# Performance work log

Hardware: AMD Instinct MI355X
Metric: run time of the kernel (lower is better)

## Reference

```python
import jax, jax.numpy as jnp
import numpy as np

DELTA_V = 0.5
DELTA_D = 3.0
ALPHA = 1.0
BETA = 1.0
GAMMA = 0.001
K = 5  # max instance label (labels 1..K; 0 = background)


def setup_inputs() -> dict:
    key = jax.random.key(0)
    k1, k2 = jax.random.split(key)
    B, D, H, W = 8, 8, 512, 1024
    embedding = jax.random.normal(k1, (B, D, H, W), dtype=jnp.float32)
    instance_mask = jax.random.randint(k2, (B, H, W), 0, K + 1, dtype=jnp.int32)
    return {"embedding": embedding, "instance_mask": instance_mask}


def _disc_loss(embedding, instance_mask):
    B, D, H, W = embedding.shape
    P = H * W
    emb = embedding.transpose(0, 2, 3, 1).reshape(B, P, D)      # [B,P,D]
    labels = instance_mask.reshape(B, P)                         # [B,P]

    # one-hot over instance labels 1..K (background excluded)
    onehot = (labels[..., None] == jnp.arange(1, K + 1, dtype=labels.dtype)).astype(emb.dtype)  # [B,P,K]
    counts = onehot.sum(axis=1)                                  # [B,K]
    present = counts > 0                                         # [B,K]
    presentf = present.astype(emb.dtype)
    N = presentf.sum(axis=-1)                                    # [B] num instances

    # per-instance centers via segment mean
    sums = jnp.einsum('bpd,bpk->bkd', emb, onehot)               # [B,K,D]
    centers = sums / jnp.maximum(counts, 1.0)[..., None]         # [B,K,D]

    # ---- variance loss: per-pixel distance to own center ----
    idx = jnp.clip(labels - 1, 0, K - 1)                         # [B,P]
    c_pix = jnp.take_along_axis(centers, idx[..., None], axis=1) # [B,P,D]
    d = jnp.sqrt(jnp.sum((emb - c_pix) ** 2, axis=-1))           # [B,P]
    val = jnp.maximum(d - DELTA_V, 0.0) ** 2                     # [B,P]
    inst_sum = jnp.einsum('bp,bpk->bk', val, onehot)             # [B,K]
    inst_mean = inst_sum / jnp.maximum(counts, 1.0)
    loss_var_b = (inst_mean * presentf).sum(-1) / jnp.maximum(N, 1.0)  # [B]

    # ---- distance loss: pairwise center hinge ----
    diff = centers[:, :, None, :] - centers[:, None, :, :]       # [B,K,K,D]
    dist_sq = jnp.sum(diff ** 2, axis=-1)                        # [B,K,K]
    iu = jnp.triu(jnp.ones((K, K), dtype=bool), k=1)             # i<j
    pair_mask = present[:, :, None] & present[:, None, :] & iu   # [B,K,K]
    safe_dist = jnp.sqrt(jnp.where(pair_mask, dist_sq, 1.0))
    term = jnp.maximum(2.0 * DELTA_D - safe_dist, 0.0) ** 2 * pair_mask.astype(emb.dtype)
    n_pairs = N * (N - 1.0) / 2.0
    loss_dist_b = term.sum((-1, -2)) / jnp.where(N > 1, n_pairs, 1.0)  # [B]

    # ---- regularization: mean norm of present centers ----
    c_norm = jnp.sqrt(jnp.where(present, jnp.sum(centers ** 2, axis=-1), 1.0))
    loss_reg_b = (c_norm * presentf).sum(-1) / jnp.maximum(N, 1.0)     # [B]

    # ---- batch mean over images that have at least one instance ----
    has = (N > 0).astype(emb.dtype)                              # [B]
    denom = jnp.maximum(has.sum(), 1.0)
    loss_var = (loss_var_b * has).sum() / denom
    loss_dist = (loss_dist_b * has).sum() / denom
    loss_reg = (loss_reg_b * has).sum() / denom
    total = ALPHA * loss_var + BETA * loss_dist + GAMMA * loss_reg
    return (total, loss_var, loss_dist, loss_reg)


def reference(embedding, instance_mask):
    return _disc_loss(embedding, instance_mask)
```

## Files before the change

kernel.cpp:

```cpp
#include <hip/hip_runtime.h>
#include <math.h>

constexpr int NB   = 8;
constexpr int ND   = 8;
constexpr int NH   = 512;
constexpr int NW   = 1024;
constexpr int NP   = NH * NW;
constexpr int NG   = NP / 4;
constexpr int NK   = 5;
constexpr int BPB  = 128;
constexpr int GPB  = NG / BPB;
constexpr int NVAL = NK * ND + NK;

constexpr float DELTA_V = 0.5f;
constexpr float TWO_DELTA_D = 6.0f;
constexpr float GAMMA = 0.001f;

__device__ __forceinline__ float wave_sum(float v) {
#pragma unroll
    for (int off = 32; off > 0; off >>= 1) v += __shfl_down(v, off, 64);
    return v;
}

__global__ __launch_bounds__(256) void pass1_kernel(const float* __restrict__ emb,
                                                    const int* __restrict__ mask,
                                                    float* __restrict__ sums,
                                                    float* __restrict__ cnts) {
    const int b   = blockIdx.x / BPB;
    const int blk = blockIdx.x % BPB;
    const long base = (long)blk * GPB;

    const float4* emb4 = (const float4*)emb;
    const int4*   m4p  = (const int4*)mask + (long)b * NG;

    float acc[NK][ND];
    float cnt[NK];
#pragma unroll
    for (int k = 0; k < NK; ++k) {
        cnt[k] = 0.f;
#pragma unroll
        for (int d = 0; d < ND; ++d) acc[k][d] = 0.f;
    }

    for (int it = threadIdx.x; it < GPB; it += blockDim.x) {
        const long g = base + it;
        const int4 m = m4p[g];
        float4 e[ND];
#pragma unroll
        for (int d = 0; d < ND; ++d)
            e[d] = emb4[((long)(b * ND + d)) * NG + g];
        const int labs[4] = {m.x, m.y, m.z, m.w};
#pragma unroll
        for (int j = 0; j < 4; ++j) {
            const int lab = labs[j];
#pragma unroll
            for (int k = 0; k < NK; ++k) {
                const float is = (lab == k + 1) ? 1.f : 0.f;
                cnt[k] += is;
#pragma unroll
                for (int d = 0; d < ND; ++d)
                    acc[k][d] = fmaf(is, ((const float*)&e[d])[j], acc[k][d]);
            }
        }
    }

    __shared__ float part[4][NVAL];
    const int lane = threadIdx.x & 63;
    const int wave = threadIdx.x >> 6;
#pragma unroll
    for (int k = 0; k < NK; ++k) {
#pragma unroll
        for (int d = 0; d < ND; ++d) {
            const float r = wave_sum(acc[k][d]);
            if (lane == 0) part[wave][k * ND + d] = r;
        }
        const float rc = wave_sum(cnt[k]);
        if (lane == 0) part[wave][NK * ND + k] = rc;
    }
    __syncthreads();
    if (threadIdx.x < NVAL) {
        const float s = part[0][threadIdx.x] + part[1][threadIdx.x] +
                        part[2][threadIdx.x] + part[3][threadIdx.x];
        if (threadIdx.x < NK * ND)
            atomicAdd(&sums[b * NK * ND + threadIdx.x], s);
        else
            atomicAdd(&cnts[b * NK + (threadIdx.x - NK * ND)], s);
    }
}

__global__ __launch_bounds__(256) void pass2_kernel(const float* __restrict__ emb,
                                                    const int* __restrict__ mask,
                                                    const float* __restrict__ sums,
                                                    const float* __restrict__ cnts,
                                                    float* __restrict__ vsums) {
    const int b   = blockIdx.x / BPB;
    const int blk = blockIdx.x % BPB;
    const long base = (long)blk * GPB;

    float c[NK][ND];
#pragma unroll
    for (int k = 0; k < NK; ++k) {
        const float inv = 1.f / fmaxf(cnts[b * NK + k], 1.f);
#pragma unroll
        for (int d = 0; d < ND; ++d)
            c[k][d] = sums[b * NK * ND + k * ND + d] * inv;
    }

    const float4* emb4 = (const float4*)emb;
    const int4*   m4p  = (const int4*)mask + (long)b * NG;

    float vacc[NK] = {0.f, 0.f, 0.f, 0.f, 0.f};

    for (int it = threadIdx.x; it < GPB; it += blockDim.x) {
        const long g = base + it;
        const int4 m = m4p[g];
        float4 e[ND];
#pragma unroll
        for (int d = 0; d < ND; ++d)
            e[d] = emb4[((long)(b * ND + d)) * NG + g];
        const int labs[4] = {m.x, m.y, m.z, m.w};
#pragma unroll
        for (int j = 0; j < 4; ++j) {
            const int lab = labs[j];
            float dsq = 0.f;
#pragma unroll
            for (int d = 0; d < ND; ++d) {
                float cd = c[0][d];
                cd = (lab == 2) ? c[1][d] : cd;
                cd = (lab == 3) ? c[2][d] : cd;
                cd = (lab == 4) ? c[3][d] : cd;
                cd = (lab == 5) ? c[4][d] : cd;
                const float diff = ((const float*)&e[d])[j] - cd;
                dsq = fmaf(diff, diff, dsq);
            }
            const float dist = sqrtf(dsq);
            float hv = fmaxf(dist - DELTA_V, 0.f);
            const float val = hv * hv;
#pragma unroll
            for (int k = 0; k < NK; ++k)
                vacc[k] += (lab == k + 1) ? val : 0.f;
        }
    }

    __shared__ float part[4][NK];
    const int lane = threadIdx.x & 63;
    const int wave = threadIdx.x >> 6;
#pragma unroll
    for (int k = 0; k < NK; ++k) {
        const float r = wave_sum(vacc[k]);
        if (lane == 0) part[wave][k] = r;
    }
    __syncthreads();
    if (threadIdx.x < NK) {
        const float s = part[0][threadIdx.x] + part[1][threadIdx.x] +
                        part[2][threadIdx.x] + part[3][threadIdx.x];
        atomicAdd(&vsums[b * NK + threadIdx.x], s);
    }
}

__global__ void final_kernel(const float* __restrict__ sums,
                             const float* __restrict__ cnts,
                             const float* __restrict__ vsums,
                             float* __restrict__ out) {
    if (threadIdx.x != 0 || blockIdx.x != 0) return;
    float tv = 0.f, td = 0.f, tr = 0.f, hs = 0.f;
    for (int b = 0; b < NB; ++b) {
        float cnt[NK];
        bool  pres[NK];
        float c[NK][ND];
        float N = 0.f;
        for (int k = 0; k < NK; ++k) {
            cnt[k]  = cnts[b * NK + k];
            pres[k] = cnt[k] > 0.f;
            if (pres[k]) N += 1.f;
            const float inv = 1.f / fmaxf(cnt[k], 1.f);
            for (int d = 0; d < ND; ++d)
                c[k][d] = sums[b * NK * ND + k * ND + d] * inv;
        }
        float lv = 0.f;
        for (int k = 0; k < NK; ++k)
            if (pres[k]) lv += vsums[b * NK + k] / fmaxf(cnt[k], 1.f);
        lv /= fmaxf(N, 1.f);
        float ld = 0.f;
        for (int i = 0; i < NK; ++i)
            for (int j = i + 1; j < NK; ++j)
                if (pres[i] && pres[j]) {
                    float dsq = 0.f;
                    for (int d = 0; d < ND; ++d) {
                        const float df = c[i][d] - c[j][d];
                        dsq = fmaf(df, df, dsq);
                    }
                    const float t = fmaxf(TWO_DELTA_D - sqrtf(dsq), 0.f);
                    ld += t * t;
                }
        const float npairs = N * (N - 1.f) * 0.5f;
        ld /= (N > 1.f) ? npairs : 1.f;
        float lr = 0.f;
        for (int k = 0; k < NK; ++k)
            if (pres[k]) {
                float sq = 0.f;
                for (int d = 0; d < ND; ++d) sq = fmaf(c[k][d], c[k][d], sq);
                lr += sqrtf(sq);
            }
        lr /= fmaxf(N, 1.f);

        if (N > 0.f) { tv += lv; td += ld; tr += lr; hs += 1.f; }
    }
    const float denom = fmaxf(hs, 1.f);
    tv /= denom; td /= denom; tr /= denom;
    out[0] = tv + td + GAMMA * tr;
    out[1] = tv;
    out[2] = td;
    out[3] = tr;
}

extern "C" void kernel_launch(void* const* d_in, const int* in_sizes, int n_in,
                              void* d_out, int out_size, void* d_ws, size_t ws_size,
                              hipStream_t stream) {
    const float* emb  = (const float*)d_in[0];
    const int*   mask = (const int*)d_in[1];
    float* out = (float*)d_out;

    float* sums  = (float*)d_ws;
    float* cnts  = sums + NB * NK * ND;
    float* vsums = cnts + NB * NK;

    hipMemsetAsync(d_ws, 0, (size_t)(NB * NK * ND + 2 * NB * NK) * sizeof(float), stream);

    dim3 grid(NB * BPB), block(256);
    pass1_kernel<<<grid, block, 0, stream>>>(emb, mask, sums, cnts);
    pass2_kernel<<<grid, block, 0, stream>>>(emb, mask, sums, cnts, vsums);
    final_kernel<<<1, 64, 0, stream>>>(sums, cnts, vsums, out);
}
```

Baseline: 284.2 us.

## Fuse both passes and finalization into one persistent kernel with grid barriers

Replaces the memset plus three kernel launches with a single 512-block kernel. Block 0 zeroes the workspace in-kernel, and the other blocks wait on a ready flag. Software grid barriers separate the center-accumulation pass, the variance pass and the final scalar reduction, and the pixel loops are fully unrolled with a fixed trip count. The aim is to remove launch and memset overhead and to let the second read of the embedding hit the on-chip caches. In exchange it relies on all blocks being co-resident. The ready flag persists across calls, so a later call could race with the workspace reset.

```diff
diff --git a/kernel.cpp b/kernel.cpp
--- a/kernel.cpp
+++ b/kernel.cpp
@@ -1,20 +1,24 @@
 #include <hip/hip_runtime.h>
 #include <math.h>
 
-constexpr int NB   = 8;
-constexpr int ND   = 8;
-constexpr int NH   = 512;
-constexpr int NW   = 1024;
-constexpr int NP   = NH * NW;
-constexpr int NG   = NP / 4;
-constexpr int NK   = 5;
-constexpr int BPB  = 128;
+constexpr int NB = 8, ND = 8, NH = 512, NW = 1024;
+constexpr int NP = NH * NW;
+constexpr int NG = NP / 4;
+constexpr int NK = 5;
+constexpr int NBLK = 512;
+constexpr int BPB  = NBLK / NB;
 constexpr int GPB  = NG / BPB;
+constexpr int ITER = GPB / 256;
 constexpr int NVAL = NK * ND + NK;
 
 constexpr float DELTA_V = 0.5f;
 constexpr float TWO_DELTA_D = 6.0f;
 constexpr float GAMMA = 0.001f;
+constexpr int READY_MAGIC = 0x13572468;
+
+#define SCOPE __HIP_MEMORY_SCOPE_AGENT
+
+constexpr int WS_INTS = 416;
 
 __device__ __forceinline__ float wave_sum(float v) {
 #pragma unroll
@@ -22,19 +26,48 @@
     return v;
 }
 
-__global__ __launch_bounds__(256) void pass1_kernel(const float* __restrict__ emb,
-                                                    const int* __restrict__ mask,
-                                                    float* __restrict__ sums,
-                                                    float* __restrict__ cnts) {
+__device__ __forceinline__ void grid_barrier(int* cnt, int* gen) {
+    __syncthreads();
+    if (threadIdx.x == 0) {
+        const int g = __hip_atomic_load(gen, __ATOMIC_ACQUIRE, SCOPE);
+        const int t = __hip_atomic_fetch_add(cnt, 1, __ATOMIC_ACQ_REL, SCOPE);
+        if (t == NBLK - 1) {
+            __hip_atomic_store(cnt, 0, __ATOMIC_RELAXED, SCOPE);
+            __hip_atomic_fetch_add(gen, 1, __ATOMIC_ACQ_REL, SCOPE);
+        } else {
+            while (__hip_atomic_load(gen, __ATOMIC_ACQUIRE, SCOPE) == g)
+                __builtin_amdgcn_s_sleep(2);
+        }
+    }
+    __syncthreads();
+}
+
+__global__ __launch_bounds__(256, 2) void disc_fused(
+    const float* __restrict__ emb, const int* __restrict__ mask,
+    int* __restrict__ wsi, float* __restrict__ out)
+{
+    float* const sums    = (float*)(wsi + 16);
+    float* const cnts    = sums + NB * NK * ND;
+    float* const vsums   = cnts + NB * NK;
+    int* const   bar_cnt = wsi + 0;
+    int* const   bar_gen = wsi + 1;
+    int* const   ready   = wsi + 2;
+
     const int b   = blockIdx.x / BPB;
     const int blk = blockIdx.x % BPB;
     const long base = (long)blk * GPB;
-
-    const float4* emb4 = (const float4*)emb;
+    const float4* emb4 = (const float4*)emb + (long)b * ND * NG;
     const int4*   m4p  = (const int4*)mask + (long)b * NG;
 
-    float acc[NK][ND];
-    float cnt[NK];
+    if (blockIdx.x == 0) {
+        for (int i = threadIdx.x; i < WS_INTS; i += 256)
+            __hip_atomic_store(wsi + i, 0, __ATOMIC_RELAXED, SCOPE);
+        __syncthreads();
+        if (threadIdx.x == 0)
+            __hip_atomic_store(ready, READY_MAGIC, __ATOMIC_RELEASE, SCOPE);
+    }
+
+    float acc[NK][ND], cnt[NK];
 #pragma unroll
     for (int k = 0; k < NK; ++k) {
         cnt[k] = 0.f;
@@ -42,24 +75,24 @@
         for (int d = 0; d < ND; ++d) acc[k][d] = 0.f;
     }
 
-    for (int it = threadIdx.x; it < GPB; it += blockDim.x) {
-        const long g = base + it;
+#pragma unroll
+    for (int i = 0; i < ITER; ++i) {
+        const long g = base + threadIdx.x + i * 256;
         const int4 m = m4p[g];
         float4 e[ND];
 #pragma unroll
-        for (int d = 0; d < ND; ++d)
-            e[d] = emb4[((long)(b * ND + d)) * NG + g];
+        for (int d = 0; d < ND; ++d) e[d] = emb4[(long)d * NG + g];
         const int labs[4] = {m.x, m.y, m.z, m.w};
 #pragma unroll
         for (int j = 0; j < 4; ++j) {
             const int lab = labs[j];
 #pragma unroll
             for (int k = 0; k < NK; ++k) {
-                const float is = (lab == k + 1) ? 1.f : 0.f;
-                cnt[k] += is;
+                const bool sel = (lab == k + 1);
+                cnt[k] += sel ? 1.f : 0.f;
 #pragma unroll
                 for (int d = 0; d < ND; ++d)
-                    acc[k][d] = fmaf(is, ((const float*)&e[d])[j], acc[k][d]);
+                    acc[k][d] += sel ? ((const float*)&e[d])[j] : 0.f;
             }
         }
     }
@@ -77,47 +110,45 @@
         const float rc = wave_sum(cnt[k]);
         if (lane == 0) part[wave][NK * ND + k] = rc;
     }
+    if (threadIdx.x == 0 && blockIdx.x != 0) {
+        while (__hip_atomic_load(ready, __ATOMIC_ACQUIRE, SCOPE) != READY_MAGIC)
+            __builtin_amdgcn_s_sleep(2);
+    }
     __syncthreads();
     if (threadIdx.x < NVAL) {
         const float s = part[0][threadIdx.x] + part[1][threadIdx.x] +
                         part[2][threadIdx.x] + part[3][threadIdx.x];
-        if (threadIdx.x < NK * ND)
-            atomicAdd(&sums[b * NK * ND + threadIdx.x], s);
-        else
-            atomicAdd(&cnts[b * NK + (threadIdx.x - NK * ND)], s);
-    }
-}
-
-__global__ __launch_bounds__(256) void pass2_kernel(const float* __restrict__ emb,
-                                                    const int* __restrict__ mask,
-                                                    const float* __restrict__ sums,
-                                                    const float* __restrict__ cnts,
-                                                    float* __restrict__ vsums) {
-    const int b   = blockIdx.x / BPB;
-    const int blk = blockIdx.x % BPB;
-    const long base = (long)blk * GPB;
-
+        float* dst = (threadIdx.x < NK * ND)
+                         ? &sums[b * NK * ND + threadIdx.x]
+                         : &cnts[b * NK + (threadIdx.x - NK * ND)];
+        atomicAdd(dst, s);
+    }
+    grid_barrier(bar_cnt, bar_gen);
+
+    __shared__ float csh[NVAL];
+    if (threadIdx.x < NVAL) {
+        const float* src = (threadIdx.x < NK * ND)
+                               ? &sums[b * NK * ND + threadIdx.x]
+                               : &cnts[b * NK + (threadIdx.x - NK * ND)];
+        csh[threadIdx.x] = __hip_atomic_load(src, __ATOMIC_RELAXED, SCOPE);
+    }
+    __syncthreads();
     float c[NK][ND];
 #pragma unroll
     for (int k = 0; k < NK; ++k) {
-        const float inv = 1.f / fmaxf(cnts[b * NK + k], 1.f);
-#pragma unroll
-        for (int d = 0; d < ND; ++d)
-            c[k][d] = sums[b * NK * ND + k * ND + d] * inv;
-    }
-
-    const float4* emb4 = (const float4*)emb;
-    const int4*   m4p  = (const int4*)mask + (long)b * NG;
+        const float inv = 1.f / fmaxf(csh[NK * ND + k], 1.f);
+#pragma unroll
+        for (int d = 0; d < ND; ++d) c[k][d] = csh[k * ND + d] * inv;
+    }
 
     float vacc[NK] = {0.f, 0.f, 0.f, 0.f, 0.f};
-
-    for (int it = threadIdx.x; it < GPB; it += blockDim.x) {
-        const long g = base + it;
+#pragma unroll
+    for (int i = 0; i < ITER; ++i) {
+        const long g = base + threadIdx.x + i * 256;
         const int4 m = m4p[g];
         float4 e[ND];
 #pragma unroll
-        for (int d = 0; d < ND; ++d)
-            e[d] = emb4[((long)(b * ND + d)) * NG + g];
+        for (int d = 0; d < ND; ++d) e[d] = emb4[(long)d * NG + g];
         const int labs[4] = {m.x, m.y, m.z, m.w};
 #pragma unroll
         for (int j = 0; j < 4; ++j) {
@@ -134,17 +165,13 @@
                 dsq = fmaf(diff, diff, dsq);
             }
             const float dist = sqrtf(dsq);
-            float hv = fmaxf(dist - DELTA_V, 0.f);
+            const float hv = fmaxf(dist - DELTA_V, 0.f);
             const float val = hv * hv;
 #pragma unroll
             for (int k = 0; k < NK; ++k)
                 vacc[k] += (lab == k + 1) ? val : 0.f;
         }
     }
-
-    __shared__ float part[4][NK];
-    const int lane = threadIdx.x & 63;
-    const int wave = threadIdx.x >> 6;
 #pragma unroll
     for (int k = 0; k < NK; ++k) {
         const float r = wave_sum(vacc[k]);
@@ -156,62 +183,63 @@
                         part[2][threadIdx.x] + part[3][threadIdx.x];
         atomicAdd(&vsums[b * NK + threadIdx.x], s);
     }
-}
-
-__global__ void final_kernel(const float* __restrict__ sums,
-                             const float* __restrict__ cnts,
-                             const float* __restrict__ vsums,
-                             float* __restrict__ out) {
-    if (threadIdx.x != 0 || blockIdx.x != 0) return;
-    float tv = 0.f, td = 0.f, tr = 0.f, hs = 0.f;
-    for (int b = 0; b < NB; ++b) {
-        float cnt[NK];
-        bool  pres[NK];
-        float c[NK][ND];
-        float N = 0.f;
-        for (int k = 0; k < NK; ++k) {
-            cnt[k]  = cnts[b * NK + k];
-            pres[k] = cnt[k] > 0.f;
-            if (pres[k]) N += 1.f;
-            const float inv = 1.f / fmaxf(cnt[k], 1.f);
-            for (int d = 0; d < ND; ++d)
-                c[k][d] = sums[b * NK * ND + k * ND + d] * inv;
-        }
-        float lv = 0.f;
-        for (int k = 0; k < NK; ++k)
-            if (pres[k]) lv += vsums[b * NK + k] / fmaxf(cnt[k], 1.f);
-        lv /= fmaxf(N, 1.f);
-        float ld = 0.f;
-        for (int i = 0; i < NK; ++i)
-            for (int j = i + 1; j < NK; ++j)
-                if (pres[i] && pres[j]) {
-                    float dsq = 0.f;
-                    for (int d = 0; d < ND; ++d) {
-                        const float df = c[i][d] - c[j][d];
-                        dsq = fmaf(df, df, dsq);
+    grid_barrier(bar_cnt, bar_gen);
+
+    if (blockIdx.x == 0 && threadIdx.x == 0) {
+        float tv = 0.f, td = 0.f, tr = 0.f, hs = 0.f;
+        for (int bb = 0; bb < NB; ++bb) {
+            float cc[NK], CC[NK][ND];
+            bool pres[NK];
+            float N = 0.f;
+            for (int k = 0; k < NK; ++k) {
+                cc[k] = __hip_atomic_load(&cnts[bb * NK + k], __ATOMIC_RELAXED, SCOPE);
+                pres[k] = cc[k] > 0.f;
+                if (pres[k]) N += 1.f;
+                const float inv = 1.f / fmaxf(cc[k], 1.f);
+                for (int d = 0; d < ND; ++d)
+                    CC[k][d] = __hip_atomic_load(&sums[bb * NK * ND + k * ND + d],
+                                                 __ATOMIC_RELAXED, SCOPE) * inv;
+            }
+            float lv = 0.f;
+            for (int k = 0; k < NK; ++k)
+                if (pres[k])
+                    lv += __hip_atomic_load(&vsums[bb * NK + k], __ATOMIC_RELAXED, SCOPE)
+                          / fmaxf(cc[k], 1.f);
+            lv /= fmaxf(N, 1.f);
+
+            float ld = 0.f;
+            for (int i2 = 0; i2 < NK; ++i2)
+                for (int j2 = i2 + 1; j2 < NK; ++j2)
+                    if (pres[i2] && pres[j2]) {
+                        float dsq = 0.f;
+                        for (int d = 0; d < ND; ++d) {
+                            const float df = CC[i2][d] - CC[j2][d];
+                            dsq = fmaf(df, df, dsq);
+                        }
+                        const float t = fmaxf(TWO_DELTA_D - sqrtf(dsq), 0.f);
+                        ld += t * t;
                     }
-                    const float t = fmaxf(TWO_DELTA_D - sqrtf(dsq), 0.f);
-                    ld += t * t;
+            const float npairs = N * (N - 1.f) * 0.5f;
+            ld /= (N > 1.f) ? npairs : 1.f;
+
+            float lr = 0.f;
+            for (int k = 0; k < NK; ++k)
+                if (pres[k]) {
+                    float sq = 0.f;
+                    for (int d = 0; d < ND; ++d) sq = fmaf(CC[k][d], CC[k][d], sq);
+                    lr += sqrtf(sq);
                 }
-        const float npairs = N * (N - 1.f) * 0.5f;
-        ld /= (N > 1.f) ? npairs : 1.f;
-        float lr = 0.f;
-        for (int k = 0; k < NK; ++k)
-            if (pres[k]) {
-                float sq = 0.f;
-                for (int d = 0; d < ND; ++d) sq = fmaf(c[k][d], c[k][d], sq);
-                lr += sqrtf(sq);
-            }
-        lr /= fmaxf(N, 1.f);
-
-        if (N > 0.f) { tv += lv; td += ld; tr += lr; hs += 1.f; }
-    }
-    const float denom = fmaxf(hs, 1.f);
-    tv /= denom; td /= denom; tr /= denom;
-    out[0] = tv + td + GAMMA * tr;
-    out[1] = tv;
-    out[2] = td;
-    out[3] = tr;
+            lr /= fmaxf(N, 1.f);
+
+            if (N > 0.f) { tv += lv; td += ld; tr += lr; hs += 1.f; }
+        }
+        const float den = fmaxf(hs, 1.f);
+        tv /= den; td /= den; tr /= den;
+        out[0] = tv + td + GAMMA * tr;
+        out[1] = tv;
+        out[2] = td;
+        out[3] = tr;
+    }
 }
 
 extern "C" void kernel_launch(void* const* d_in, const int* in_sizes, int n_in,
@@ -219,16 +247,5 @@
                               hipStream_t stream) {
     const float* emb  = (const float*)d_in[0];
     const int*   mask = (const int*)d_in[1];
-    float* out = (float*)d_out;
-
-    float* sums  = (float*)d_ws;
-    float* cnts  = sums + NB * NK * ND;
-    float* vsums = cnts + NB * NK;
-
-    hipMemsetAsync(d_ws, 0, (size_t)(NB * NK * ND + 2 * NB * NK) * sizeof(float), stream);
-
-    dim3 grid(NB * BPB), block(256);
-    pass1_kernel<<<grid, block, 0, stream>>>(emb, mask, sums, cnts);
-    pass2_kernel<<<grid, block, 0, stream>>>(emb, mask, sums, cnts, vsums);
-    final_kernel<<<1, 64, 0, stream>>>(sums, cnts, vsums, out);
-}
+    disc_fused<<<dim3(NBLK), dim3(256), 0, stream>>>(emb, mask, (int*)d_ws, (float*)d_out);
+}
```

After: 523.2 us. 1.84x slower.
